# Optimization experiments

Measured on AMD Instinct MI355X. Metric: run time of the kernel, lower is better.

Reference implementation:

```python
import jax, jax.numpy as jnp
import numpy as np

B, D, K, N = 32, 512, 64, 1024
EPS = 1e-12  # torch F.normalize eps


def setup_inputs() -> dict:
    key = jax.random.key(0)
    k1, k2, k3 = jax.random.split(key, 3)
    x = jax.random.normal(k1, (B, D, N), dtype=jnp.float32)
    conv_w = jax.random.normal(k2, (K, D), dtype=jnp.float32) * (1.0 / np.sqrt(D))
    centers = jax.random.normal(k3, (D, K), dtype=jnp.float32)
    return {"x": x, "conv_w": conv_w, "centers": centers}


def reference(x, conv_w, centers):
    # scores: 1x1 conv over flattened spatial dim -> [B, K, N]
    scores = jnp.einsum('kd,bdn->bkn', conv_w, x)
    assign = jax.nn.softmax(scores, axis=1)                 # softmax over clusters
    # Algebraic rewrite of sum_n assign[b,k,n] * (x[b,d,n] - centers[d,k]):
    vlad = (jnp.einsum('bdn,bkn->bdk', x, assign)
            - centers[None, :, :] * assign.sum(axis=-1)[:, None, :])  # [B, D, K]
    # intra-normalization over descriptor dim D (F.normalize with eps clamp)
    vlad = vlad / jnp.maximum(jnp.linalg.norm(vlad, axis=1, keepdims=True), EPS)
    desc = vlad.reshape(vlad.shape[0], -1)                  # [B, D*K]
    desc = desc / jnp.maximum(jnp.linalg.norm(desc, axis=1, keepdims=True), EPS)
    return desc
```

## Files before the change

### kernel.cpp

```cpp
#include <hip/hip_runtime.h>
#include <hip/hip_bf16.h>

#define Bv 32
#define Dv 512
#define Kv 64
#define Nv 1024
#define EPSv 1e-12f

typedef __attribute__((ext_vector_type(8))) short bf16x8;
typedef __attribute__((ext_vector_type(4))) float f32x4;

__device__ __forceinline__ unsigned short f2b(float f) {
  union { float f; unsigned u; } v; v.f = f;
  unsigned r = v.u + 0x7fffu + ((v.u >> 16) & 1u);
  return (unsigned short)(r >> 16);
}
__device__ __forceinline__ unsigned pack2(float a, float b) {
  return (unsigned)f2b(a) | ((unsigned)f2b(b) << 16);
}

__global__ __launch_bounds__(256) void wconv(const float* __restrict__ w,
                                             unsigned short* __restrict__ wbf) {
  int i = (blockIdx.x * 256 + threadIdx.x) * 4;
  float4 v = *(const float4*)&w[i];
  uint2 o = make_uint2(pack2(v.x, v.y), pack2(v.z, v.w));
  *(uint2*)&wbf[i] = o;
}

__global__ __launch_bounds__(512) void fused_scores(
    const float* __restrict__ x, const unsigned short* __restrict__ wbf,
    unsigned short* __restrict__ xbf, unsigned short* __restrict__ assign,
    float* __restrict__ asum) {
  __shared__ unsigned short xT[64 * 520];
  __shared__ float redmax[4][64];
  __shared__ float redsum[4][64];

  const int t = threadIdx.x;
  const int b = blockIdx.y;
  const int nt = blockIdx.x;
  const int n0 = nt * 64;

  {
    const int lo = t & 15;
    const int hi = t >> 4;
    const int s = (lo >> 1) & 3;
    const float* xb = x + (size_t)b * Dv * Nv + n0;
    unsigned short* xt = xbf + ((size_t)b * 16 + nt) * (Dv * 64);
#pragma unroll
    for (int r = 0; r < 8; r++) {
      int d = (hi + 32 * r) * 2;
      int n4 = lo * 4;
      float4 v0 = *(const float4*)&xb[(size_t)d * Nv + n4];
      float4 v1 = *(const float4*)&xb[(size_t)(d + 1) * Nv + n4];
      *(uint2*)&xt[(size_t)d * 64 + n4] =
          make_uint2(pack2(v0.x, v0.y), pack2(v0.z, v0.w));
      *(uint2*)&xt[(size_t)(d + 1) * 64 + n4] =
          make_uint2(pack2(v1.x, v1.y), pack2(v1.z, v1.w));
      unsigned w0 = pack2(v0.x, v1.x);
      unsigned w1 = pack2(v0.y, v1.y);
      unsigned w2 = pack2(v0.z, v1.z);
      unsigned w3 = pack2(v0.w, v1.w);
      unsigned a0 = (s & 1) ? w1 : w0, a1 = (s & 1) ? w2 : w1,
               a2 = (s & 1) ? w3 : w2, a3 = (s & 1) ? w0 : w3;
      unsigned b0 = (s & 2) ? a2 : a0, b1 = (s & 2) ? a3 : a1,
               b2 = (s & 2) ? a0 : a2, b3 = (s & 2) ? a1 : a3;
      *(unsigned*)&xT[(n4 + ((0 + s) & 3)) * 520 + d] = b0;
      *(unsigned*)&xT[(n4 + ((1 + s) & 3)) * 520 + d] = b1;
      *(unsigned*)&xT[(n4 + ((2 + s) & 3)) * 520 + d] = b2;
      *(unsigned*)&xT[(n4 + ((3 + s) & 3)) * 520 + d] = b3;
    }
  }
  __syncthreads();

  const int wv = t >> 6;
  const int lane = t & 63;
  const int q = lane >> 4;
  const int m = lane & 15;
  const int k16 = wv & 3;
  const int nsub = wv >> 2;

  f32x4 acc0 = {0.f, 0.f, 0.f, 0.f};
  f32x4 acc1 = {0.f, 0.f, 0.f, 0.f};

  const unsigned short* wp = wbf + (size_t)(k16 * 16 + m) * Dv + q * 8;
  const unsigned short* l0 = &xT[(nsub * 32 + m) * 520 + q * 8];
  const unsigned short* l1 = l0 + 16 * 520;

#pragma unroll
  for (int d0 = 0; d0 < Dv; d0 += 32) {
    bf16x8 af = *(const bf16x8*)(wp + d0);
    bf16x8 bf0 = *(const bf16x8*)(l0 + d0);
    bf16x8 bf1 = *(const bf16x8*)(l1 + d0);
    acc0 = __builtin_amdgcn_mfma_f32_16x16x32_bf16(af, bf0, acc0, 0, 0, 0);
    acc1 = __builtin_amdgcn_mfma_f32_16x16x32_bf16(af, bf1, acc1, 0, 0, 0);
  }

  float m0 = fmaxf(fmaxf(acc0[0], acc0[1]), fmaxf(acc0[2], acc0[3]));
  float m1 = fmaxf(fmaxf(acc1[0], acc1[1]), fmaxf(acc1[2], acc1[3]));
  m0 = fmaxf(m0, __shfl_xor(m0, 16)); m0 = fmaxf(m0, __shfl_xor(m0, 32));
  m1 = fmaxf(m1, __shfl_xor(m1, 16)); m1 = fmaxf(m1, __shfl_xor(m1, 32));
  if (q == 0) {
    redmax[k16][nsub * 32 + m] = m0;
    redmax[k16][nsub * 32 + 16 + m] = m1;
  }
  __syncthreads();
  const int c0 = nsub * 32 + m, c1 = c0 + 16;
  float mc0 = fmaxf(fmaxf(redmax[0][c0], redmax[1][c0]), fmaxf(redmax[2][c0], redmax[3][c0]));
  float mc1 = fmaxf(fmaxf(redmax[0][c1], redmax[1][c1]), fmaxf(redmax[2][c1], redmax[3][c1]));

  float e0[4], e1[4];
  float s0 = 0.f, s1 = 0.f;
#pragma unroll
  for (int r = 0; r < 4; r++) {
    e0[r] = __expf(acc0[r] - mc0); s0 += e0[r];
    e1[r] = __expf(acc1[r] - mc1); s1 += e1[r];
  }
  s0 += __shfl_xor(s0, 16); s0 += __shfl_xor(s0, 32);
  s1 += __shfl_xor(s1, 16); s1 += __shfl_xor(s1, 32);
  if (q == 0) {
    redsum[k16][c0] = s0;
    redsum[k16][c1] = s1;
  }
  __syncthreads();
  float sc0 = 1.0f / (redsum[0][c0] + redsum[1][c0] + redsum[2][c0] + redsum[3][c0]);
  float sc1 = 1.0f / (redsum[0][c1] + redsum[1][c1] + redsum[2][c1] + redsum[3][c1]);

  unsigned short* at_ = assign + ((size_t)b * 16 + nt) * (Kv * 64)
                        + (size_t)(k16 * 16 + q * 4) * 64 + nsub * 32;
#pragma unroll
  for (int r = 0; r < 4; r++) {
    float v0 = e0[r] * sc0;
    float v1 = e1[r] * sc1;
    at_[r * 64 + m] = f2b(v0);
    at_[r * 64 + 16 + m] = f2b(v1);
    float p = v0 + v1;
    p += __shfl_xor(p, 1); p += __shfl_xor(p, 2);
    p += __shfl_xor(p, 4); p += __shfl_xor(p, 8);
    if (m == 0) atomicAdd(&asum[b * Kv + k16 * 16 + q * 4 + r], p);
  }
}

__global__ __launch_bounds__(512, 2) void vlad_mfma(
    const unsigned short* __restrict__ xbf, const unsigned short* __restrict__ assign,
    const float* __restrict__ centers, const float* __restrict__ asum,
    float* __restrict__ vlad, float* __restrict__ colsq) {
  __shared__ float sred[4][64][4];

  const int t = threadIdx.x;
  const int b = blockIdx.y;
  const int d0 = blockIdx.x * 16;
  const int wv = t >> 6;
  const int ksub = wv & 3;
  const int nh = wv >> 2;
  const int lane = t & 63;
  const int q = lane >> 4;
  const int m = lane & 15;
  const int k16 = ksub * 16;

  const unsigned short* xp = xbf + ((size_t)b * 16 + nh * 8) * (Dv * 64)
                             + (size_t)(d0 + m) * 64 + q * 8;
  const unsigned short* ap = assign + ((size_t)b * 16 + nh * 8) * (Kv * 64)
                             + (size_t)(k16 + m) * 64 + q * 8;

  f32x4 acc = {0.f, 0.f, 0.f, 0.f};
  bf16x8 xv[8], av[8];

#pragma unroll
  for (int i = 0; i < 8; i++) {
    xv[i] = *(const bf16x8*)(xp + (i >> 1) * (Dv * 64) + (i & 1) * 32);
    av[i] = *(const bf16x8*)(ap + (i >> 1) * (Kv * 64) + (i & 1) * 32);
  }
  __builtin_amdgcn_sched_barrier(0);

#pragma unroll
  for (int i = 0; i < 8; i++) {
    acc = __builtin_amdgcn_mfma_f32_16x16x32_bf16(xv[i], av[i], acc, 0, 0, 0);
    xv[i] = *(const bf16x8*)(xp + ((i + 8) >> 1) * (Dv * 64) + (i & 1) * 32);
    av[i] = *(const bf16x8*)(ap + ((i + 8) >> 1) * (Kv * 64) + (i & 1) * 32);
    __builtin_amdgcn_sched_barrier(0);
  }

#pragma unroll
  for (int i = 0; i < 8; i++)
    acc = __builtin_amdgcn_mfma_f32_16x16x32_bf16(xv[i], av[i], acc, 0, 0, 0);

  if (nh == 1) {
#pragma unroll
    for (int r = 0; r < 4; r++) sred[ksub][lane][r] = acc[r];
  }
  __syncthreads();
  if (nh == 0) {
    const int k = k16 + m;
    const float as = asum[b * Kv + k];
    float ss = 0.f;
#pragma unroll
    for (int r = 0; r < 4; r++) {
      float v = acc[r] + sred[ksub][lane][r];
      int d = d0 + q * 4 + r;
      float val = v - centers[d * Kv + k] * as;
      vlad[((size_t)b * Dv + d) * Kv + k] = val;
      ss = fmaf(val, val, ss);
    }
    ss += __shfl_xor(ss, 16);
    ss += __shfl_xor(ss, 32);
    if (q == 0) atomicAdd(&colsq[b * Kv + k], ss);
  }
}

__global__ __launch_bounds__(256) void scale_kernel(
    const float* __restrict__ vlad, const float* __restrict__ colsq,
    float* __restrict__ out) {
  const int t = threadIdx.x;
  const size_t i = (size_t)blockIdx.x * 256 + t;
  const int b = (int)(i >> 15);
  __shared__ float scs[64];
  __shared__ float bsh;
  if (t < 64) {
    float tot = colsq[b * Kv + t];
    float sc = 1.0f / fmaxf(sqrtf(tot), EPSv);
    scs[t] = sc;
    float contrib = tot * sc * sc;
#pragma unroll
    for (int off = 32; off > 0; off >>= 1) contrib += __shfl_down(contrib, off);
    if (t == 0) bsh = 1.0f / fmaxf(sqrtf(contrib), EPSv);
  }
  __syncthreads();
  out[i] = vlad[i] * scs[i & 63] * bsh;
}

extern "C" void kernel_launch(void* const* d_in, const int* in_sizes, int n_in,
                              void* d_out, int out_size, void* d_ws, size_t ws_size,
                              hipStream_t stream) {
  const float* x = (const float*)d_in[0];
  const float* w = (const float*)d_in[1];
  const float* centers = (const float*)d_in[2];
  float* out = (float*)d_out;

  char* ws = (char*)d_ws;
  unsigned short* assign = (unsigned short*)ws;
  float* vlad = (float*)(ws + 4194304);
  unsigned short* xbf = (unsigned short*)(ws + 8388608);
  unsigned short* wbf = (unsigned short*)(ws + 41943040);
  float* asum = (float*)(ws + 42008576);
  float* colsq = asum + Bv * Kv;

  hipMemsetAsync(asum, 0, (size_t)2 * Bv * Kv * sizeof(float), stream);

  wconv<<<32, 256, 0, stream>>>(w, wbf);
  fused_scores<<<dim3(Nv / 64, Bv), 512, 0, stream>>>(x, wbf, xbf, assign, asum);
  vlad_mfma<<<dim3(Dv / 16, Bv), 512, 0, stream>>>(xbf, assign, centers, asum, vlad, colsq);
  scale_kernel<<<(Bv * Dv * Kv) / 256, 256, 0, stream>>>(vlad, colsq, out);
}
```

Baseline: 145.3 us.

## Fold memset into wconv, swizzle vlad block order, vectorize scale kernel

```diff
diff --git a/kernel.cpp b/kernel.cpp
--- a/kernel.cpp
+++ b/kernel.cpp
@@ -20,11 +20,14 @@
 }
 
 __global__ __launch_bounds__(256) void wconv(const float* __restrict__ w,
-                                             unsigned short* __restrict__ wbf) {
-  int i = (blockIdx.x * 256 + threadIdx.x) * 4;
+                                             unsigned short* __restrict__ wbf,
+                                             float* __restrict__ zbuf) {
+  int id = blockIdx.x * 256 + threadIdx.x;
+  int i = id * 4;
   float4 v = *(const float4*)&w[i];
   uint2 o = make_uint2(pack2(v.x, v.y), pack2(v.z, v.w));
   *(uint2*)&wbf[i] = o;
+  if (id < 2 * Bv * Kv) zbuf[id] = 0.f;
 }
 
 __global__ __launch_bounds__(512) void fused_scores(
@@ -147,8 +150,10 @@
   __shared__ float sred[4][64][4];
 
   const int t = threadIdx.x;
-  const int b = blockIdx.y;
-  const int d0 = blockIdx.x * 16;
+  const int flat = blockIdx.x;
+  const int loc = flat >> 3;
+  const int b = ((loc >> 5) << 3) + (flat & 7);
+  const int d0 = (loc & 31) * 16;
   const int wv = t >> 6;
   const int ksub = wv & 3;
   const int nh = wv >> 2;
@@ -211,7 +216,7 @@
     const float* __restrict__ vlad, const float* __restrict__ colsq,
     float* __restrict__ out) {
   const int t = threadIdx.x;
-  const size_t i = (size_t)blockIdx.x * 256 + t;
+  const size_t i = ((size_t)blockIdx.x * 256 + t) * 4;
   const int b = (int)(i >> 15);
   __shared__ float scs[64];
   __shared__ float bsh;
@@ -225,7 +230,14 @@
     if (t == 0) bsh = 1.0f / fmaxf(sqrtf(contrib), EPSv);
   }
   __syncthreads();
-  out[i] = vlad[i] * scs[i & 63] * bsh;
+  float4 v = *(const float4*)&vlad[i];
+  const int k = (int)(i & 63);
+  float4 o;
+  o.x = v.x * scs[k + 0] * bsh;
+  o.y = v.y * scs[k + 1] * bsh;
+  o.z = v.z * scs[k + 2] * bsh;
+  o.w = v.w * scs[k + 3] * bsh;
+  *(float4*)&out[i] = o;
 }
 
 extern "C" void kernel_launch(void* const* d_in, const int* in_sizes, int n_in,
@@ -244,10 +256,8 @@
   float* asum = (float*)(ws + 42008576);
   float* colsq = asum + Bv * Kv;
 
-  hipMemsetAsync(asum, 0, (size_t)2 * Bv * Kv * sizeof(float), stream);
-
-  wconv<<<32, 256, 0, stream>>>(w, wbf);
+  wconv<<<32, 256, 0, stream>>>(w, wbf, asum);
   fused_scores<<<dim3(Nv / 64, Bv), 512, 0, stream>>>(x, wbf, xbf, assign, asum);
-  vlad_mfma<<<dim3(Dv / 16, Bv), 512, 0, stream>>>(xbf, assign, centers, asum, vlad, colsq);
-  scale_kernel<<<(Bv * Dv * Kv) / 256, 256, 0, stream>>>(vlad, colsq, out);
-}
+  vlad_mfma<<<1024, 512, 0, stream>>>(xbf, assign, centers, asum, vlad, colsq);
+  scale_kernel<<<1024, 256, 0, stream>>>(vlad, colsq, out);
+}
```

After: 143.5 us. About the same (-1.2%).
